# Optimization experiments

Hardware: AMD Instinct MI355X
Metric: run time of the kernel (lower is better)

## Reference

```python
import jax, jax.numpy as jnp
import numpy as np

NUM_USERS = 100000
NUM_ITEMS = 50000
NUM_NODES = NUM_USERS + NUM_ITEMS
EMBED_DIM = 128
NUM_LAYERS = 3
CONTENT_DIM = 768
NUM_EDGES = 1000000
BATCH = 4096
LAMBDA_CONTENT = 0.1
INIT_STD = 0.1


def setup_inputs() -> dict:
    key = jax.random.key(0)
    ks = jax.random.split(key, 9)
    edge_index = jax.random.randint(ks[0], (2, NUM_EDGES), 0, NUM_NODES, dtype=jnp.int64 if jax.config.jax_enable_x64 else jnp.int32)
    edge_weight = jax.random.uniform(ks[1], (NUM_EDGES,), dtype=jnp.float32)
    batch_users = jax.random.randint(ks[2], (BATCH,), 0, NUM_USERS)
    batch_pos_items = jax.random.randint(ks[3], (BATCH,), 0, NUM_ITEMS)
    batch_neg_items = jax.random.randint(ks[4], (BATCH,), 0, NUM_ITEMS)
    item_content = jax.random.normal(ks[5], (NUM_ITEMS, CONTENT_DIM), dtype=jnp.float32)
    user_emb_w = INIT_STD * jax.random.normal(ks[6], (NUM_USERS, EMBED_DIM), dtype=jnp.float32)
    item_emb_w = INIT_STD * jax.random.normal(ks[7], (NUM_ITEMS, EMBED_DIM), dtype=jnp.float32)
    # nn.Linear(item_content_dim, embed_dim, bias=False): weight [embed_dim, content_dim]
    bound = 1.0 / np.sqrt(CONTENT_DIM)
    content_proj_w = jax.random.uniform(ks[8], (EMBED_DIM, CONTENT_DIM), minval=-bound, maxval=bound, dtype=jnp.float32)
    return {
        'edge_index': edge_index, 'edge_weight': edge_weight,
        'batch_users': batch_users, 'batch_pos_items': batch_pos_items,
        'batch_neg_items': batch_neg_items, 'item_content': item_content,
        'user_emb_w': user_emb_w, 'item_emb_w': item_emb_w,
        'content_proj_w': content_proj_w,
    }


def _lgconv(x, src, dst, ew, num_nodes):
    # PyG LGConv: gcn_norm(add_self_loops=False) then scatter-add at target.
    deg = jax.ops.segment_sum(ew, dst, num_segments=num_nodes)          # [N]
    dinv = jnp.where(deg > 0, jax.lax.rsqrt(deg), 0.0)
    norm = dinv[src] * ew * dinv[dst]                                    # [E]
    return jax.ops.segment_sum(norm[:, None] * x[src], dst, num_segments=num_nodes)


def _propagate(user_emb_w, item_emb_w, src, dst, ew):
    x = jnp.concatenate([user_emb_w, item_emb_w], axis=0)               # [N, D]
    acc = x
    for _ in range(NUM_LAYERS):
        x = _lgconv(x, src, dst, ew, NUM_NODES)
        acc = acc + x
    x_final = acc / (NUM_LAYERS + 1)
    return x_final[:NUM_USERS], x_final[NUM_USERS:]


def reference(edge_index, edge_weight, batch_users, batch_pos_items,
              batch_neg_items, item_content, user_emb_w, item_emb_w,
              content_proj_w):
    src, dst = edge_index[0], edge_index[1]
    u_final, i_final = _propagate(user_emb_w, item_emb_w, src, dst, edge_weight)
    u = u_final[batch_users]
    i_pos = i_final[batch_pos_items]
    i_neg = i_final[batch_neg_items]
    pos_score = jnp.sum(u * i_pos, axis=-1)
    neg_score = jnp.sum(u * i_neg, axis=-1)
    bpr = jnp.mean(jax.nn.softplus(-(pos_score - neg_score)))
    reg = jnp.mean(jnp.sum(u**2, axis=1) + jnp.sum(i_pos**2, axis=1) + jnp.sum(i_neg**2, axis=1)) * 1e-4
    proj = item_content @ content_proj_w.T                              # [I, D]
    align = jnp.mean((i_final - proj) ** 2)
    loss = bpr + reg + LAMBDA_CONTENT * align
    return loss, u_final, i_final
```

## Files before the change

kernel.cpp:

```cpp
#include <hip/hip_runtime.h>
#include <math.h>

#define NU 100000
#define NI 50000
#define NN 150000
#define D 128
#define NE 1000000
#define CD 768
#define BATCH 4096
#define NGEMM 782
#define NK (CD / 64)

typedef short bf16x8 __attribute__((ext_vector_type(8)));
typedef float f32x4 __attribute__((ext_vector_type(4)));

static inline size_t alignup(size_t x, size_t a) { return (x + a - 1) / a * a; }

__device__ inline unsigned short f2bf(float f) {
  unsigned int u = __builtin_bit_cast(unsigned int, f);
  unsigned int r = (u + 0x7fffu + ((u >> 16) & 1u)) >> 16;
  return (unsigned short)r;
}
__device__ inline unsigned int pack2bf(float lo, float hi) {
  return (unsigned int)f2bf(lo) | ((unsigned int)f2bf(hi) << 16);
}
__device__ inline float bflo(unsigned int p) {
  return __builtin_bit_cast(float, p << 16);
}
__device__ inline float bfhi(unsigned int p) {
  return __builtin_bit_cast(float, p & 0xffff0000u);
}

#define ACC8(P, W)                                                        \
  a[0] = fmaf(W, bflo(P.x), a[0]); a[1] = fmaf(W, bfhi(P.x), a[1]);       \
  a[2] = fmaf(W, bflo(P.y), a[2]); a[3] = fmaf(W, bfhi(P.y), a[3]);       \
  a[4] = fmaf(W, bflo(P.z), a[4]); a[5] = fmaf(W, bfhi(P.z), a[5]);       \
  a[6] = fmaf(W, bflo(P.w), a[6]); a[7] = fmaf(W, bfhi(P.w), a[7]);

__device__ __forceinline__ void gather_rows(
    const int* __restrict__ row_ptr, const uint2* __restrict__ cedge,
    const uint4* __restrict__ xin, int n, int sub, float* a) {
  int beg = row_ptr[n], end = row_ptr[n + 1];
  int j = beg;
  for (; j + 4 <= end; j += 4) {
    uint2 e0 = cedge[j], e1 = cedge[j + 1], e2 = cedge[j + 2], e3 = cedge[j + 3];
    uint4 p0 = xin[(size_t)e0.x * 16 + sub];
    uint4 p1 = xin[(size_t)e1.x * 16 + sub];
    uint4 p2 = xin[(size_t)e2.x * 16 + sub];
    uint4 p3 = xin[(size_t)e3.x * 16 + sub];
    float w0 = __builtin_bit_cast(float, e0.y);
    float w1 = __builtin_bit_cast(float, e1.y);
    float w2 = __builtin_bit_cast(float, e2.y);
    float w3 = __builtin_bit_cast(float, e3.y);
    ACC8(p0, w0) ACC8(p1, w1) ACC8(p2, w2) ACC8(p3, w3)
  }
  for (; j < end; ++j) {
    uint2 e0 = cedge[j];
    uint4 p0 = xin[(size_t)e0.x * 16 + sub];
    float w0 = __builtin_bit_cast(float, e0.y);
    ACC8(p0, w0)
  }
}

__global__ __launch_bounds__(512) void prep_kernel(
    const int* __restrict__ dst, int* __restrict__ cnt, int* __restrict__ cpos,
    const float* __restrict__ uemb, const float* __restrict__ iemb,
    unsigned int* __restrict__ x0b,
    const float* __restrict__ W, const float* __restrict__ content,
    uint4* __restrict__ proj) {
  __shared__ unsigned short Asm[2][64 * 64];
  __shared__ unsigned short Bsm[2][128 * 64];

  int bid = blockIdx.x;
  int tid = threadIdx.x;

  if (bid >= NGEMM) {
    int sub = bid - NGEMM;
    int half = sub >> 1;
    if ((sub & 1) == 0) {
      int i = half * 512 + tid;
      for (; i < NE; i += 1024 * 512)
        cpos[i] = atomicAdd(&cnt[dst[i]], 1);
    } else {
      const size_t XT = (size_t)NN * D / 8;
      size_t t = (size_t)half * 512 + tid;
      for (; t < XT; t += (size_t)1024 * 512) {
        size_t f = t * 8;
        const float* p = (f < (size_t)NU * D) ? (uemb + f) : (iemb + (f - (size_t)NU * D));
        float4 a = *(const float4*)p;
        float4 b = *(const float4*)(p + 4);
        uint4 o;
        o.x = pack2bf(a.x, a.y); o.y = pack2bf(a.z, a.w);
        o.z = pack2bf(b.x, b.y); o.w = pack2bf(b.z, b.w);
        *(uint4*)(x0b + t * 4) = o;
      }
    }
    return;
  }

  int w = tid >> 6, lane = tid & 63;
  int i0 = bid * 64;
  int lrow = lane & 15, kq = lane >> 4;

  f32x4 acc[4];
#pragma unroll
  for (int rt = 0; rt < 4; ++rt) acc[rt] = (f32x4){0.f, 0.f, 0.f, 0.f};

  int sr = tid >> 3, c8 = tid & 7;
  int arow_g = (i0 + sr < NI) ? (i0 + sr) : (NI - 1);
  const float* aG = content + (size_t)arow_g * CD + c8 * 8;
  const float* bG0 = W + (size_t)sr * CD + c8 * 8;
  const float* bG1 = W + (size_t)(sr + 64) * CD + c8 * 8;
  int aoff = (c8 * 16) ^ ((sr & 7) << 4);

  {
    float4 a0 = *(const float4*)(aG);
    float4 a1 = *(const float4*)(aG + 4);
    float4 p0 = *(const float4*)(bG0);
    float4 p1 = *(const float4*)(bG0 + 4);
    float4 q0 = *(const float4*)(bG1);
    float4 q1 = *(const float4*)(bG1 + 4);
    uint4 oa, ob, oc;
    oa.x = pack2bf(a0.x, a0.y); oa.y = pack2bf(a0.z, a0.w);
    oa.z = pack2bf(a1.x, a1.y); oa.w = pack2bf(a1.z, a1.w);
    ob.x = pack2bf(p0.x, p0.y); ob.y = pack2bf(p0.z, p0.w);
    ob.z = pack2bf(p1.x, p1.y); ob.w = pack2bf(p1.z, p1.w);
    oc.x = pack2bf(q0.x, q0.y); oc.y = pack2bf(q0.z, q0.w);
    oc.z = pack2bf(q1.x, q1.y); oc.w = pack2bf(q1.z, q1.w);
    *(uint4*)((char*)Asm[0] + sr * 128 + aoff) = oa;
    *(uint4*)((char*)Bsm[0] + sr * 128 + aoff) = ob;
    *(uint4*)((char*)Bsm[0] + (sr + 64) * 128 + aoff) = oc;
  }

  for (int kk = 0; kk < NK; ++kk) {
    __syncthreads();
    int cur = kk & 1, nxt = cur ^ 1;
    bool more = kk < NK - 1;
    float4 a0, a1, p0, p1, q0, q1;
    if (more) {
      int k0 = (kk + 1) * 64;
      a0 = *(const float4*)(aG + k0);
      a1 = *(const float4*)(aG + k0 + 4);
      p0 = *(const float4*)(bG0 + k0);
      p1 = *(const float4*)(bG0 + k0 + 4);
      q0 = *(const float4*)(bG1 + k0);
      q1 = *(const float4*)(bG1 + k0 + 4);
    }
#pragma unroll
    for (int ks = 0; ks < 2; ++ks) {
      int kbyte = ks * 64 + kq * 16;
      bf16x8 af[4], bfr;
#pragma unroll
      for (int rt = 0; rt < 4; ++rt) {
        int row = rt * 16 + lrow;
        af[rt] = *(const bf16x8*)((char*)Asm[cur] + row * 128 + (kbyte ^ ((row & 7) << 4)));
      }
      {
        int row = w * 16 + lrow;
        bfr = *(const bf16x8*)((char*)Bsm[cur] + row * 128 + (kbyte ^ ((row & 7) << 4)));
      }
#pragma unroll
      for (int rt = 0; rt < 4; ++rt)
        acc[rt] = __builtin_amdgcn_mfma_f32_16x16x32_bf16(af[rt], bfr, acc[rt], 0, 0, 0);
    }
    if (more) {
      uint4 oa, ob, oc;
      oa.x = pack2bf(a0.x, a0.y); oa.y = pack2bf(a0.z, a0.w);
      oa.z = pack2bf(a1.x, a1.y); oa.w = pack2bf(a1.z, a1.w);
      ob.x = pack2bf(p0.x, p0.y); ob.y = pack2bf(p0.z, p0.w);
      ob.z = pack2bf(p1.x, p1.y); ob.w = pack2bf(p1.z, p1.w);
      oc.x = pack2bf(q0.x, q0.y); oc.y = pack2bf(q0.z, q0.w);
      oc.z = pack2bf(q1.x, q1.y); oc.w = pack2bf(q1.z, q1.w);
      *(uint4*)((char*)Asm[nxt] + sr * 128 + aoff) = oa;
      *(uint4*)((char*)Bsm[nxt] + sr * 128 + aoff) = ob;
      *(uint4*)((char*)Bsm[nxt] + (sr + 64) * 128 + aoff) = oc;
    }
  }

  __syncthreads();
  unsigned short* T = (unsigned short*)Asm;
  int dcol = w * 16 + lrow;
#pragma unroll
  for (int rt = 0; rt < 4; ++rt)
#pragma unroll
    for (int j = 0; j < 4; ++j)
      T[(rt * 16 + kq * 4 + j) * 128 + dcol] = f2bf(acc[rt][j]);
  __syncthreads();
#pragma unroll
  for (int u0 = 0; u0 < 2; ++u0) {
    int u = u0 * 512 + tid;
    int r = u >> 4, s = u & 15;
    int it = i0 + r;
    if (it < NI) proj[(size_t)it * 16 + s] = ((const uint4*)T)[u];
  }
}


__global__ void scan_p1(const int* __restrict__ cnt, int* __restrict__ bsum) {
  __shared__ int s[256];
  int b = blockIdx.x;
  int i = b * 256 + threadIdx.x;
  s[threadIdx.x] = (i < NN) ? cnt[i] : 0;
  __syncthreads();
  for (int off = 128; off; off >>= 1) {
    if (threadIdx.x < off) s[threadIdx.x] += s[threadIdx.x + off];
    __syncthreads();
  }
  if (threadIdx.x == 0) bsum[b] = s[0];
}

__global__ __launch_bounds__(1024) void scan_p2(int* __restrict__ bsum, int nb) {
  __shared__ int s[1024];
  int t = threadIdx.x;
  int v = (t < nb) ? bsum[t] : 0;
  s[t] = v;
  __syncthreads();
  for (int off = 1; off < 1024; off <<= 1) {
    int u = (t >= off) ? s[t - off] : 0;
    __syncthreads();
    s[t] += u;
    __syncthreads();
  }
  if (t < nb) bsum[t] = s[t] - v;
}

__global__ void scan_p3(const int* __restrict__ cnt, const int* __restrict__ bsum,
                        int* __restrict__ row_ptr) {
  __shared__ int s[256];
  int b = blockIdx.x;
  int i = b * 256 + threadIdx.x;
  s[threadIdx.x] = (i < NN) ? cnt[i] : 0;
  __syncthreads();
  for (int off = 1; off < 256; off <<= 1) {
    int t = (threadIdx.x >= off) ? s[threadIdx.x - off] : 0;
    __syncthreads();
    s[threadIdx.x] += t;
    __syncthreads();
  }
  if (i < NN) row_ptr[i + 1] = bsum[b] + s[threadIdx.x];
  if (i == 0) row_ptr[0] = 0;
}

__global__ void fill_kernel(const int* __restrict__ src, const int* __restrict__ dst,
                            const float* __restrict__ ew, const int* __restrict__ row_ptr,
                            const int* __restrict__ cpos, uint2* __restrict__ cedge) {
  int i = blockIdx.x * blockDim.x + threadIdx.x;
  int stride = gridDim.x * blockDim.x;
  for (; i < NE; i += stride) {
    int p = row_ptr[dst[i]] + cpos[i];
    uint2 e;
    e.x = (unsigned int)src[i];
    e.y = __builtin_bit_cast(unsigned int, ew[i]);
    cedge[p] = e;
  }
}

__global__ void degrow_kernel(const int* __restrict__ row_ptr, const uint2* __restrict__ cedge,
                              float* __restrict__ dinv) {
  int n = blockIdx.x * blockDim.x + threadIdx.x;
  if (n >= NN) return;
  int beg = row_ptr[n], end = row_ptr[n + 1];
  float s = 0.f;
  for (int p = beg; p < end; ++p) s += __builtin_bit_cast(float, cedge[p].y);
  dinv[n] = (s > 0.f) ? rsqrtf(s) : 0.f;
}

__global__ void norm_kernel(uint2* __restrict__ cedge, const float* __restrict__ dinv) {
  int i = blockIdx.x * blockDim.x + threadIdx.x;
  int stride = gridDim.x * blockDim.x;
  for (; i < NE; i += stride) {
    uint2 e = cedge[i];
    float nm = dinv[e.x] * __builtin_bit_cast(float, e.y);
    cedge[i].y = __builtin_bit_cast(unsigned int, nm);
  }
}

__global__ __launch_bounds__(256) void gather_kernel(
    const int* __restrict__ row_ptr, const uint2* __restrict__ cedge,
    const float* __restrict__ dinv, const uint4* __restrict__ xin,
    uint4* __restrict__ yout) {
  int tid = threadIdx.x;
  int wv = tid >> 6, lane = tid & 63;
  int g = lane >> 4, sub = lane & 15;
  int n = blockIdx.x * 16 + wv * 4 + g;
  if (n >= NN) return;
  float a[8] = {0.f, 0.f, 0.f, 0.f, 0.f, 0.f, 0.f, 0.f};
  gather_rows(row_ptr, cedge, xin, n, sub, a);
  float sc = dinv[n];
  uint4 o;
  o.x = pack2bf(a[0] * sc, a[1] * sc);
  o.y = pack2bf(a[2] * sc, a[3] * sc);
  o.z = pack2bf(a[4] * sc, a[5] * sc);
  o.w = pack2bf(a[6] * sc, a[7] * sc);
  yout[(size_t)n * 16 + sub] = o;
}

__global__ __launch_bounds__(256) void final_kernel(
    const int* __restrict__ row_ptr, const uint2* __restrict__ cedge,
    const float* __restrict__ dinv, const uint4* __restrict__ x0b,
    const uint4* __restrict__ y1b, const uint4* __restrict__ y2b,
    const uint4* __restrict__ proj, float* __restrict__ OUT,
    float* __restrict__ partials) {
  __shared__ float wred[4];
  int tid = threadIdx.x;
  int wv = tid >> 6, lane = tid & 63;
  int g = lane >> 4, sub = lane & 15;
  int n = blockIdx.x * 16 + wv * 4 + g;
  if (n >= NN) return;
  float a[8] = {0.f, 0.f, 0.f, 0.f, 0.f, 0.f, 0.f, 0.f};
  gather_rows(row_ptr, cedge, y2b, n, sub, a);
  float sc = dinv[n];
  size_t r = (size_t)n * 16 + sub;
  uint4 q0 = x0b[r], q1 = y1b[r], q2 = y2b[r];
  float v[8];
  v[0] = (bflo(q0.x) + bflo(q1.x) + bflo(q2.x) + a[0] * sc) * 0.25f;
  v[1] = (bfhi(q0.x) + bfhi(q1.x) + bfhi(q2.x) + a[1] * sc) * 0.25f;
  v[2] = (bflo(q0.y) + bflo(q1.y) + bflo(q2.y) + a[2] * sc) * 0.25f;
  v[3] = (bfhi(q0.y) + bfhi(q1.y) + bfhi(q2.y) + a[3] * sc) * 0.25f;
  v[4] = (bflo(q0.z) + bflo(q1.z) + bflo(q2.z) + a[4] * sc) * 0.25f;
  v[5] = (bfhi(q0.z) + bfhi(q1.z) + bfhi(q2.z) + a[5] * sc) * 0.25f;
  v[6] = (bflo(q0.w) + bflo(q1.w) + bflo(q2.w) + a[6] * sc) * 0.25f;
  v[7] = (bfhi(q0.w) + bfhi(q1.w) + bfhi(q2.w) + a[7] * sc) * 0.25f;
  float* op = OUT + (size_t)n * D + sub * 8;
#pragma unroll
  for (int k = 0; k < 8; ++k) op[k] = v[k];

  if (blockIdx.x >= (NU / 16)) {
    uint4 pj = proj[(size_t)(n - NU) * 16 + sub];
    float d0 = v[0] - bflo(pj.x), d1 = v[1] - bfhi(pj.x);
    float d2 = v[2] - bflo(pj.y), d3 = v[3] - bfhi(pj.y);
    float d4 = v[4] - bflo(pj.z), d5 = v[5] - bfhi(pj.z);
    float d6 = v[6] - bflo(pj.w), d7 = v[7] - bfhi(pj.w);
    float m = d0 * d0 + d1 * d1 + d2 * d2 + d3 * d3 + d4 * d4 + d5 * d5 + d6 * d6 + d7 * d7;
    for (int off = 32; off; off >>= 1) m += __shfl_down(m, off);
    if (lane == 0) wred[wv] = m;
    __syncthreads();
    if (tid == 0)
      atomicAdd(&partials[blockIdx.x & 255], wred[0] + wred[1] + wred[2] + wred[3]);
  }
}

__global__ __launch_bounds__(256) void loss_batch(
    const int* __restrict__ bu, const int* __restrict__ bp, const int* __restrict__ bn,
    const float* __restrict__ OUT, float* __restrict__ accums) {
  __shared__ float wsp[4], wrg[4];
  int wv = threadIdx.x >> 6, lane = threadIdx.x & 63;
  int gw = blockIdx.x * 4 + wv;
  int nw = gridDim.x * 4;
  float lsp = 0.f, lrg = 0.f;
  for (int b = gw; b < BATCH; b += nw) {
    const float* u = OUT + (size_t)bu[b] * D;
    const float* ip = OUT + ((size_t)NU + bp[b]) * D;
    const float* in_ = OUT + ((size_t)NU + bn[b]) * D;
    float u0 = u[lane], u1 = u[lane + 64];
    float p0 = ip[lane], p1 = ip[lane + 64];
    float n0 = in_[lane], n1 = in_[lane + 64];
    float ps = u0 * p0 + u1 * p1;
    float ns = u0 * n0 + u1 * n1;
    float rg = u0 * u0 + u1 * u1 + p0 * p0 + p1 * p1 + n0 * n0 + n1 * n1;
    for (int off = 32; off; off >>= 1) {
      ps += __shfl_down(ps, off);
      ns += __shfl_down(ns, off);
      rg += __shfl_down(rg, off);
    }
    if (lane == 0) {
      float x = ns - ps;
      lsp += fmaxf(x, 0.f) + log1pf(expf(-fabsf(x)));
      lrg += rg;
    }
  }
  if (lane == 0) { wsp[wv] = lsp; wrg[wv] = lrg; }
  __syncthreads();
  if (threadIdx.x == 0) {
    atomicAdd(&accums[0], wsp[0] + wsp[1] + wsp[2] + wsp[3]);
    atomicAdd(&accums[1], wrg[0] + wrg[1] + wrg[2] + wrg[3]);
  }
}

__global__ void finalize_kernel(const float* __restrict__ accums,
                                const float* __restrict__ partials,
                                float* __restrict__ out0) {
  __shared__ float sm[4];
  int tid = threadIdx.x;
  float v = partials[tid];
  for (int off = 32; off; off >>= 1) v += __shfl_down(v, off);
  if ((tid & 63) == 0) sm[tid >> 6] = v;
  __syncthreads();
  if (tid == 0) {
    float align_sum = sm[0] + sm[1] + sm[2] + sm[3];
    float bpr = accums[0] / (float)BATCH;
    float reg = (accums[1] / (float)BATCH) * 1e-4f;
    float align = align_sum / (float)((size_t)NI * D);
    out0[0] = bpr + reg + 0.1f * align;
  }
}

extern "C" void kernel_launch(void* const* d_in, const int* in_sizes, int n_in,
                              void* d_out, int out_size, void* d_ws, size_t ws_size,
                              hipStream_t stream) {
  const int* edge_index = (const int*)d_in[0];
  const float* ew = (const float*)d_in[1];
  const int* bu = (const int*)d_in[2];
  const int* bp = (const int*)d_in[3];
  const int* bn = (const int*)d_in[4];
  const float* content = (const float*)d_in[5];
  const float* uemb = (const float*)d_in[6];
  const float* iemb = (const float*)d_in[7];
  const float* W = (const float*)d_in[8];
  const int* src = edge_index;
  const int* dst = edge_index + NE;
  float* outf = (float*)d_out;
  float* OUT = outf + 1;

  char* ws = (char*)d_ws;
  size_t off = 0;
  auto alloc = [&](size_t bytes) {
    void* p = ws + off;
    off = alignup(off + bytes, 256);
    return p;
  };
  unsigned int* x0b = (unsigned int*)alloc((size_t)NN * 64 * 4);
  unsigned int* y1b = (unsigned int*)alloc((size_t)NN * 64 * 4);
  unsigned int* y2b = (unsigned int*)alloc((size_t)NN * 64 * 4);
  uint4* proj = (uint4*)alloc((size_t)NI * 16 * 16);
  float* dinv = (float*)alloc((size_t)NN * 4);
  int* cnt = (int*)alloc((size_t)NN * 4);
  int* row_ptr = (int*)alloc((size_t)(NN + 1) * 4);
  int NB = (NN + 255) / 256;
  int* bsum = (int*)alloc((size_t)NB * 4);
  int* cpos = (int*)alloc((size_t)NE * 4);
  uint2* cedge = (uint2*)alloc((size_t)NE * 8);
  float* accums = (float*)alloc(16 + 256 * 4);
  float* partials = accums + 4;

  hipMemsetAsync(cnt, 0, (size_t)NN * 4, stream);
  hipMemsetAsync(accums, 0, 16 + 256 * 4, stream);

  prep_kernel<<<NGEMM + 2048, 512, 0, stream>>>(dst, cnt, cpos, uemb, iemb, x0b, W, content, proj);
  scan_p1<<<NB, 256, 0, stream>>>(cnt, bsum);
  scan_p2<<<1, 1024, 0, stream>>>(bsum, NB);
  scan_p3<<<NB, 256, 0, stream>>>(cnt, bsum, row_ptr);
  fill_kernel<<<2048, 256, 0, stream>>>(src, dst, ew, row_ptr, cpos, cedge);
  degrow_kernel<<<NB, 256, 0, stream>>>(row_ptr, cedge, dinv);
  norm_kernel<<<2048, 256, 0, stream>>>(cedge, dinv);

  int LB = (NN + 15) / 16;
  gather_kernel<<<LB, 256, 0, stream>>>(row_ptr, cedge, dinv, (const uint4*)x0b, (uint4*)y1b);
  gather_kernel<<<LB, 256, 0, stream>>>(row_ptr, cedge, dinv, (const uint4*)y1b, (uint4*)y2b);
  final_kernel<<<LB, 256, 0, stream>>>(row_ptr, cedge, dinv,
                                       (const uint4*)x0b, (const uint4*)y1b, (const uint4*)y2b,
                                       proj, OUT, partials);

  loss_batch<<<64, 256, 0, stream>>>(bu, bp, bn, OUT, accums);
  finalize_kernel<<<1, 256, 0, stream>>>(accums, partials, outf);
}
```

Baseline: 322.2 us.

## Split content GEMM out of prep kernel and pre-convert W to bf16

```diff
diff --git a/kernel.cpp b/kernel.cpp
--- a/kernel.cpp
+++ b/kernel.cpp
@@ -62,29 +62,23 @@
   }
 }
 
-__global__ __launch_bounds__(512) void prep_kernel(
+__global__ __launch_bounds__(256) void prep_kernel(
     const int* __restrict__ dst, int* __restrict__ cnt, int* __restrict__ cpos,
     const float* __restrict__ uemb, const float* __restrict__ iemb,
     unsigned int* __restrict__ x0b,
-    const float* __restrict__ W, const float* __restrict__ content,
-    uint4* __restrict__ proj) {
-  __shared__ unsigned short Asm[2][64 * 64];
-  __shared__ unsigned short Bsm[2][128 * 64];
-
-  int bid = blockIdx.x;
+    const float* __restrict__ W, unsigned short* __restrict__ Wb) {
+  int half = blockIdx.x >> 1;
   int tid = threadIdx.x;
-
-  if (bid >= NGEMM) {
-    int sub = bid - NGEMM;
-    int half = sub >> 1;
-    if ((sub & 1) == 0) {
-      int i = half * 512 + tid;
-      for (; i < NE; i += 1024 * 512)
-        cpos[i] = atomicAdd(&cnt[dst[i]], 1);
-    } else {
-      const size_t XT = (size_t)NN * D / 8;
-      size_t t = (size_t)half * 512 + tid;
-      for (; t < XT; t += (size_t)1024 * 512) {
+  if ((blockIdx.x & 1) == 0) {
+    int i = half * 256 + tid;
+    for (; i < NE; i += 2048 * 256)
+      cpos[i] = atomicAdd(&cnt[dst[i]], 1);
+  } else {
+    const size_t XT = (size_t)NN * D / 8;
+    const size_t WT = (size_t)D * CD / 8;
+    size_t t = (size_t)half * 256 + tid;
+    for (; t < XT + WT; t += (size_t)2048 * 256) {
+      if (t < XT) {
         size_t f = t * 8;
         const float* p = (f < (size_t)NU * D) ? (uemb + f) : (iemb + (f - (size_t)NU * D));
         float4 a = *(const float4*)p;
@@ -93,105 +87,16 @@
         o.x = pack2bf(a.x, a.y); o.y = pack2bf(a.z, a.w);
         o.z = pack2bf(b.x, b.y); o.w = pack2bf(b.z, b.w);
         *(uint4*)(x0b + t * 4) = o;
+      } else {
+        size_t f = (t - XT) * 8;
+        float4 a = *(const float4*)(W + f);
+        float4 b = *(const float4*)(W + f + 4);
+        uint4 o;
+        o.x = pack2bf(a.x, a.y); o.y = pack2bf(a.z, a.w);
+        o.z = pack2bf(b.x, b.y); o.w = pack2bf(b.z, b.w);
+        *(uint4*)(Wb + f) = o;
       }
     }
-    return;
-  }
-
-  int w = tid >> 6, lane = tid & 63;
-  int i0 = bid * 64;
-  int lrow = lane & 15, kq = lane >> 4;
-
-  f32x4 acc[4];
-#pragma unroll
-  for (int rt = 0; rt < 4; ++rt) acc[rt] = (f32x4){0.f, 0.f, 0.f, 0.f};
-
-  int sr = tid >> 3, c8 = tid & 7;
-  int arow_g = (i0 + sr < NI) ? (i0 + sr) : (NI - 1);
-  const float* aG = content + (size_t)arow_g * CD + c8 * 8;
-  const float* bG0 = W + (size_t)sr * CD + c8 * 8;
-  const float* bG1 = W + (size_t)(sr + 64) * CD + c8 * 8;
-  int aoff = (c8 * 16) ^ ((sr & 7) << 4);
-
-  {
-    float4 a0 = *(const float4*)(aG);
-    float4 a1 = *(const float4*)(aG + 4);
-    float4 p0 = *(const float4*)(bG0);
-    float4 p1 = *(const float4*)(bG0 + 4);
-    float4 q0 = *(const float4*)(bG1);
-    float4 q1 = *(const float4*)(bG1 + 4);
-    uint4 oa, ob, oc;
-    oa.x = pack2bf(a0.x, a0.y); oa.y = pack2bf(a0.z, a0.w);
-    oa.z = pack2bf(a1.x, a1.y); oa.w = pack2bf(a1.z, a1.w);
-    ob.x = pack2bf(p0.x, p0.y); ob.y = pack2bf(p0.z, p0.w);
-    ob.z = pack2bf(p1.x, p1.y); ob.w = pack2bf(p1.z, p1.w);
-    oc.x = pack2bf(q0.x, q0.y); oc.y = pack2bf(q0.z, q0.w);
-    oc.z = pack2bf(q1.x, q1.y); oc.w = pack2bf(q1.z, q1.w);
-    *(uint4*)((char*)Asm[0] + sr * 128 + aoff) = oa;
-    *(uint4*)((char*)Bsm[0] + sr * 128 + aoff) = ob;
-    *(uint4*)((char*)Bsm[0] + (sr + 64) * 128 + aoff) = oc;
-  }
-
-  for (int kk = 0; kk < NK; ++kk) {
-    __syncthreads();
-    int cur = kk & 1, nxt = cur ^ 1;
-    bool more = kk < NK - 1;
-    float4 a0, a1, p0, p1, q0, q1;
-    if (more) {
-      int k0 = (kk + 1) * 64;
-      a0 = *(const float4*)(aG + k0);
-      a1 = *(const float4*)(aG + k0 + 4);
-      p0 = *(const float4*)(bG0 + k0);
-      p1 = *(const float4*)(bG0 + k0 + 4);
-      q0 = *(const float4*)(bG1 + k0);
-      q1 = *(const float4*)(bG1 + k0 + 4);
-    }
-#pragma unroll
-    for (int ks = 0; ks < 2; ++ks) {
-      int kbyte = ks * 64 + kq * 16;
-      bf16x8 af[4], bfr;
-#pragma unroll
-      for (int rt = 0; rt < 4; ++rt) {
-        int row = rt * 16 + lrow;
-        af[rt] = *(const bf16x8*)((char*)Asm[cur] + row * 128 + (kbyte ^ ((row & 7) << 4)));
-      }
-      {
-        int row = w * 16 + lrow;
-        bfr = *(const bf16x8*)((char*)Bsm[cur] + row * 128 + (kbyte ^ ((row & 7) << 4)));
-      }
-#pragma unroll
-      for (int rt = 0; rt < 4; ++rt)
-        acc[rt] = __builtin_amdgcn_mfma_f32_16x16x32_bf16(af[rt], bfr, acc[rt], 0, 0, 0);
-    }
-    if (more) {
-      uint4 oa, ob, oc;
-      oa.x = pack2bf(a0.x, a0.y); oa.y = pack2bf(a0.z, a0.w);
-      oa.z = pack2bf(a1.x, a1.y); oa.w = pack2bf(a1.z, a1.w);
-      ob.x = pack2bf(p0.x, p0.y); ob.y = pack2bf(p0.z, p0.w);
-      ob.z = pack2bf(p1.x, p1.y); ob.w = pack2bf(p1.z, p1.w);
-      oc.x = pack2bf(q0.x, q0.y); oc.y = pack2bf(q0.z, q0.w);
-      oc.z = pack2bf(q1.x, q1.y); oc.w = pack2bf(q1.z, q1.w);
-      *(uint4*)((char*)Asm[nxt] + sr * 128 + aoff) = oa;
-      *(uint4*)((char*)Bsm[nxt] + sr * 128 + aoff) = ob;
-      *(uint4*)((char*)Bsm[nxt] + (sr + 64) * 128 + aoff) = oc;
-    }
-  }
-
-  __syncthreads();
-  unsigned short* T = (unsigned short*)Asm;
-  int dcol = w * 16 + lrow;
-#pragma unroll
-  for (int rt = 0; rt < 4; ++rt)
-#pragma unroll
-    for (int j = 0; j < 4; ++j)
-      T[(rt * 16 + kq * 4 + j) * 128 + dcol] = f2bf(acc[rt][j]);
-  __syncthreads();
-#pragma unroll
-  for (int u0 = 0; u0 < 2; ++u0) {
-    int u = u0 * 512 + tid;
-    int r = u >> 4, s = u & 15;
-    int it = i0 + r;
-    if (it < NI) proj[(size_t)it * 16 + s] = ((const uint4*)T)[u];
   }
 }
 
@@ -275,6 +180,97 @@
   }
 }
 
+__global__ __launch_bounds__(512) void gemm_kernel(
+    const unsigned short* __restrict__ Wb, const float* __restrict__ content,
+    uint4* __restrict__ proj) {
+  __shared__ unsigned short Asm[2][64 * 64];
+  __shared__ unsigned short Bsm[2][128 * 64];
+
+  int tid = threadIdx.x;
+  int w = tid >> 6, lane = tid & 63;
+  int i0 = blockIdx.x * 64;
+  int lrow = lane & 15, kq = lane >> 4;
+
+  f32x4 acc[4];
+#pragma unroll
+  for (int rt = 0; rt < 4; ++rt) acc[rt] = (f32x4){0.f, 0.f, 0.f, 0.f};
+
+  int sr = tid >> 3, c8 = tid & 7;
+  int arow_g = (i0 + sr < NI) ? (i0 + sr) : (NI - 1);
+  const float* aG = content + (size_t)arow_g * CD + c8 * 8;
+  const unsigned short* bG0 = Wb + (size_t)sr * CD + c8 * 8;
+  const unsigned short* bG1 = Wb + (size_t)(sr + 64) * CD + c8 * 8;
+  int aoff = (c8 * 16) ^ ((sr & 7) << 4);
+
+  {
+    float4 a0 = *(const float4*)(aG);
+    float4 a1 = *(const float4*)(aG + 4);
+    uint4 oa;
+    oa.x = pack2bf(a0.x, a0.y); oa.y = pack2bf(a0.z, a0.w);
+    oa.z = pack2bf(a1.x, a1.y); oa.w = pack2bf(a1.z, a1.w);
+    *(uint4*)((char*)Asm[0] + sr * 128 + aoff) = oa;
+    *(uint4*)((char*)Bsm[0] + sr * 128 + aoff) = *(const uint4*)(bG0);
+    *(uint4*)((char*)Bsm[0] + (sr + 64) * 128 + aoff) = *(const uint4*)(bG1);
+  }
+
+  for (int kk = 0; kk < NK; ++kk) {
+    __syncthreads();
+    int cur = kk & 1, nxt = cur ^ 1;
+    bool more = kk < NK - 1;
+    float4 a0, a1;
+    uint4 nb0, nb1;
+    if (more) {
+      int k0 = (kk + 1) * 64;
+      a0 = *(const float4*)(aG + k0);
+      a1 = *(const float4*)(aG + k0 + 4);
+      nb0 = *(const uint4*)(bG0 + k0);
+      nb1 = *(const uint4*)(bG1 + k0);
+    }
+#pragma unroll
+    for (int ks = 0; ks < 2; ++ks) {
+      int kbyte = ks * 64 + kq * 16;
+      bf16x8 af[4], bfr;
+#pragma unroll
+      for (int rt = 0; rt < 4; ++rt) {
+        int row = rt * 16 + lrow;
+        af[rt] = *(const bf16x8*)((char*)Asm[cur] + row * 128 + (kbyte ^ ((row & 7) << 4)));
+      }
+      {
+        int row = w * 16 + lrow;
+        bfr = *(const bf16x8*)((char*)Bsm[cur] + row * 128 + (kbyte ^ ((row & 7) << 4)));
+      }
+#pragma unroll
+      for (int rt = 0; rt < 4; ++rt)
+        acc[rt] = __builtin_amdgcn_mfma_f32_16x16x32_bf16(af[rt], bfr, acc[rt], 0, 0, 0);
+    }
+    if (more) {
+      uint4 oa;
+      oa.x = pack2bf(a0.x, a0.y); oa.y = pack2bf(a0.z, a0.w);
+      oa.z = pack2bf(a1.x, a1.y); oa.w = pack2bf(a1.z, a1.w);
+      *(uint4*)((char*)Asm[nxt] + sr * 128 + aoff) = oa;
+      *(uint4*)((char*)Bsm[nxt] + sr * 128 + aoff) = nb0;
+      *(uint4*)((char*)Bsm[nxt] + (sr + 64) * 128 + aoff) = nb1;
+    }
+  }
+
+  __syncthreads();
+  unsigned short* T = (unsigned short*)Asm;
+  int dcol = w * 16 + lrow;
+#pragma unroll
+  for (int rt = 0; rt < 4; ++rt)
+#pragma unroll
+    for (int j = 0; j < 4; ++j)
+      T[(rt * 16 + kq * 4 + j) * 128 + dcol] = f2bf(acc[rt][j]);
+  __syncthreads();
+#pragma unroll
+  for (int u0 = 0; u0 < 2; ++u0) {
+    int u = u0 * 512 + tid;
+    int r = u >> 4, s = u & 15;
+    int it = i0 + r;
+    if (it < NI) proj[(size_t)it * 16 + s] = ((const uint4*)T)[u];
+  }
+}
+
 __global__ __launch_bounds__(256) void gather_kernel(
     const int* __restrict__ row_ptr, const uint2* __restrict__ cedge,
     const float* __restrict__ dinv, const uint4* __restrict__ xin,
@@ -284,9 +280,9 @@
   int g = lane >> 4, sub = lane & 15;
   int n = blockIdx.x * 16 + wv * 4 + g;
   if (n >= NN) return;
+  float sc = dinv[n];
   float a[8] = {0.f, 0.f, 0.f, 0.f, 0.f, 0.f, 0.f, 0.f};
   gather_rows(row_ptr, cedge, xin, n, sub, a);
-  float sc = dinv[n];
   uint4 o;
   o.x = pack2bf(a[0] * sc, a[1] * sc);
   o.y = pack2bf(a[2] * sc, a[3] * sc);
@@ -307,11 +303,11 @@
   int g = lane >> 4, sub = lane & 15;
   int n = blockIdx.x * 16 + wv * 4 + g;
   if (n >= NN) return;
+  size_t r = (size_t)n * 16 + sub;
+  uint4 q0 = x0b[r], q1 = y1b[r], q2 = y2b[r];
+  float sc = dinv[n];
   float a[8] = {0.f, 0.f, 0.f, 0.f, 0.f, 0.f, 0.f, 0.f};
   gather_rows(row_ptr, cedge, y2b, n, sub, a);
-  float sc = dinv[n];
-  size_t r = (size_t)n * 16 + sub;
-  uint4 q0 = x0b[r], q1 = y1b[r], q2 = y2b[r];
   float v[8];
   v[0] = (bflo(q0.x) + bflo(q1.x) + bflo(q2.x) + a[0] * sc) * 0.25f;
   v[1] = (bfhi(q0.x) + bfhi(q1.x) + bfhi(q2.x) + a[1] * sc) * 0.25f;
@@ -423,6 +419,7 @@
   unsigned int* y1b = (unsigned int*)alloc((size_t)NN * 64 * 4);
   unsigned int* y2b = (unsigned int*)alloc((size_t)NN * 64 * 4);
   uint4* proj = (uint4*)alloc((size_t)NI * 16 * 16);
+  unsigned short* Wb = (unsigned short*)alloc((size_t)D * CD * 2);
   float* dinv = (float*)alloc((size_t)NN * 4);
   int* cnt = (int*)alloc((size_t)NN * 4);
   int* row_ptr = (int*)alloc((size_t)(NN + 1) * 4);
@@ -436,7 +433,7 @@
   hipMemsetAsync(cnt, 0, (size_t)NN * 4, stream);
   hipMemsetAsync(accums, 0, 16 + 256 * 4, stream);
 
-  prep_kernel<<<NGEMM + 2048, 512, 0, stream>>>(dst, cnt, cpos, uemb, iemb, x0b, W, content, proj);
+  prep_kernel<<<4096, 256, 0, stream>>>(dst, cnt, cpos, uemb, iemb, x0b, W, Wb);
   scan_p1<<<NB, 256, 0, stream>>>(cnt, bsum);
   scan_p2<<<1, 1024, 0, stream>>>(bsum, NB);
   scan_p3<<<NB, 256, 0, stream>>>(cnt, bsum, row_ptr);
@@ -444,6 +441,8 @@
   degrow_kernel<<<NB, 256, 0, stream>>>(row_ptr, cedge, dinv);
   norm_kernel<<<2048, 256, 0, stream>>>(cedge, dinv);
 
+  gemm_kernel<<<NGEMM, 512, 0, stream>>>(Wb, content, proj);
+
   int LB = (NN + 15) / 16;
   gather_kernel<<<LB, 256, 0, stream>>>(row_ptr, cedge, dinv, (const uint4*)x0b, (uint4*)y1b);
   gather_kernel<<<LB, 256, 0, stream>>>(row_ptr, cedge, dinv, (const uint4*)y1b, (uint4*)y2b);
```

Result: slower. 344.3 us (+6.8%).
